# Kernel tuning notes

Hardware: AMD Instinct MI355X
Metric: run time of the kernel (lower is better)

The kernel has to match this reference:

```python
import jax, jax.numpy as jnp
import numpy as np

B, S, D, H = 4, 2048, 768, 12
HD = D // H  # head_dim = 64
NEG = 1e10
EPS = 1e-5

def setup_inputs() -> dict:
    key = jax.random.key(0)
    k1, k2, k3 = jax.random.split(key, 3)
    return {
        "context": jax.random.normal(k1, (B, S, D), dtype=jnp.float32),
        "pad_mask": jnp.ones((B, S), dtype=jnp.float32),
        "w_qkv": jax.random.normal(k2, (D, 3 * D), dtype=jnp.float32) * 0.02,
        "w_proj": jax.random.normal(k3, (D, D), dtype=jnp.float32) * (0.02 / np.sqrt(2.0 * 12)),
        "b_proj": jnp.zeros((D,), dtype=jnp.float32),
        "gamma": jnp.ones((D,), dtype=jnp.float32),
        "beta": jnp.zeros((D,), dtype=jnp.float32),
    }

def reference(context, pad_mask, w_qkv, w_proj, b_proj, gamma, beta):
    b, s, d = context.shape
    resid = context
    qkv = context @ w_qkv                       # [B,S,3D]
    q, k, v = jnp.split(qkv, 3, axis=-1)
    # [B,S,D] -> [B,H,S,HD]
    q = q.reshape(b, s, H, HD).transpose(0, 2, 1, 3)
    k = k.reshape(b, s, H, HD).transpose(0, 2, 1, 3)
    v = v.reshape(b, s, H, HD).transpose(0, 2, 1, 3)
    scores = jnp.einsum("bhqd,bhkd->bhqk", q, k) * (1.0 / np.sqrt(HD))
    m = pad_mask[:, None, None, :]              # [B,1,1,S]
    scores = scores * m - (1.0 - m) * NEG       # multiplicative mask + big negative
    attn = jax.nn.softmax(scores, axis=-1)      # dropout is identity at inference
    out = jnp.einsum("bhqk,bhkd->bhqd", attn, v)
    out = out.transpose(0, 2, 1, 3).reshape(b, s, d)
    out = out @ w_proj + b_proj
    x = out + resid
    mu = jnp.mean(x, axis=-1, keepdims=True)
    var = jnp.var(x, axis=-1, keepdims=True)
    return (x - mu) * jax.lax.rsqrt(var + EPS) * gamma + beta
```

## Files before the change

### kernel.cpp

```cpp
#include <hip/hip_runtime.h>

#define BB 4
#define SS 2048
#define DD 768
#define HH 12
#define HDD 64
#define BS (BB*SS)
#define NQKV (3*DD)
#define NEL (BS*DD)

typedef __attribute__((ext_vector_type(8))) __bf16 bf16x8;
typedef __attribute__((ext_vector_type(4))) float fx4;
typedef __attribute__((ext_vector_type(4))) int   ix4;

#define MFMA16(a,b,c) __builtin_amdgcn_mfma_f32_16x16x32_bf16((a),(b),(c),0,0,0)

#define GLLDS(g, l) __builtin_amdgcn_global_load_lds( \
    (const __attribute__((address_space(1))) void*)(g), \
    (__attribute__((address_space(3))) void*)(l), 16, 0, 0)

__device__ __forceinline__ unsigned short f2bf(float f) {
  unsigned u = __builtin_bit_cast(unsigned, f);
  u = (u + 0x7FFFu + ((u >> 16) & 1u)) >> 16;
  return (unsigned short)u;
}
__device__ __forceinline__ unsigned pkbf(float a, float b) {
  unsigned ua = __builtin_bit_cast(unsigned, a);
  unsigned ub = __builtin_bit_cast(unsigned, b);
  return ((ua + 0x8000u) >> 16) | ((ub + 0x8000u) & 0xFFFF0000u);
}
__device__ __forceinline__ unsigned cvtpk(float a, float b) {
  unsigned r;
  asm("v_cvt_pk_bf16_f32 %0, %1, %2" : "=v"(r) : "v"(a), "v"(b));
  return r;
}
__device__ __forceinline__ float ex2(float x) { return __builtin_amdgcn_exp2f(x); }

__global__ __launch_bounds__(256) void pack_bf16(const float* __restrict__ x,
                                                 unsigned short* __restrict__ y, int n4) {
  int i = blockIdx.x * 256 + threadIdx.x;
  if (i < n4) {
    float4 v = ((const float4*)x)[i];
    ((uint2*)y)[i] = make_uint2(pkbf(v.x, v.y), pkbf(v.z, v.w));
  }
}

__global__ __launch_bounds__(256) void pack_transpose(const float* __restrict__ w,
                                                      unsigned short* __restrict__ wT,
                                                      int K, int N) {
  __shared__ unsigned short t[32][33];
  int n0 = blockIdx.x * 32, k0 = blockIdx.y * 32;
  int tx = threadIdx.x & 31, ty = threadIdx.x >> 5;
#pragma unroll
  for (int r = ty; r < 32; r += 8)
    t[tx][r] = f2bf(w[(size_t)(k0 + r) * N + n0 + tx]);
  __syncthreads();
#pragma unroll
  for (int r = ty; r < 32; r += 8)
    wT[(size_t)(n0 + r) * K + k0 + tx] = t[r][tx];
}

__global__ __launch_bounds__(256) void gemm_qkv_k(const unsigned short* __restrict__ Wt,
                                                  const unsigned short* __restrict__ X,
                                                  unsigned short* __restrict__ Qo,
                                                  unsigned short* __restrict__ Ko,
                                                  unsigned short* __restrict__ Vto) {
  __shared__ unsigned short As[128 * 32];
  __shared__ unsigned short Bs[128 * 32];
  const int tid = threadIdx.x;
  const int w = tid >> 6, lane = tid & 63, quad = lane >> 4, l16 = lane & 15;
  const int m0 = blockIdx.y << 7;
  const int n0 = blockIdx.x << 7;
  const int wm = (w & 1) * 64, wn = (w >> 1) * 64;
  fx4 acc[4][4];
#pragma unroll
  for (int i = 0; i < 4; ++i)
#pragma unroll
    for (int c = 0; c < 4; ++c) acc[i][c] = (fx4){0.f, 0.f, 0.f, 0.f};

  const int c0 = tid, c1 = 256 + tid;
  const unsigned short* Ag0 = Wt + (size_t)(m0 + (c0 >> 2)) * DD + (c0 & 3) * 8;
  const unsigned short* Ag1 = Wt + (size_t)(m0 + (c1 >> 2)) * DD + (c1 & 3) * 8;
  const unsigned short* Bg0 = X + (size_t)(n0 + (c0 >> 2)) * DD + (c0 & 3) * 8;
  const unsigned short* Bg1 = X + (size_t)(n0 + (c1 >> 2)) * DD + (c1 & 3) * 8;
  const int wb = w * 1024;

  for (int k0 = 0; k0 < DD; k0 += 32) {
    GLLDS(Ag0 + k0, (char*)As + wb);
    GLLDS(Ag1 + k0, (char*)As + 4096 + wb);
    GLLDS(Bg0 + k0, (char*)Bs + wb);
    GLLDS(Bg1 + k0, (char*)Bs + 4096 + wb);
    __syncthreads();
    bf16x8 af[4], bf[4];
#pragma unroll
    for (int i = 0; i < 4; ++i) af[i] = *(const bf16x8*)&As[(wm + i * 16 + l16) * 32 + quad * 8];
#pragma unroll
    for (int c = 0; c < 4; ++c) bf[c] = *(const bf16x8*)&Bs[(wn + c * 16 + l16) * 32 + quad * 8];
#pragma unroll
    for (int i = 0; i < 4; ++i)
#pragma unroll
      for (int c = 0; c < 4; ++c) acc[i][c] = MFMA16(af[i], bf[c], acc[i][c]);
    __syncthreads();
  }

  const int which = m0 / DD;
#pragma unroll
  for (int i = 0; i < 4; ++i) {
    int fb = m0 + wm + i * 16 + quad * 4;
    int d = fb - which * DD;
    int h = d >> 6, hd = d & 63;
#pragma unroll
    for (int c = 0; c < 4; ++c) {
      int srow = n0 + wn + c * 16 + l16;
      int b = srow >> 11, s = srow & (SS - 1);
      if (which == 0) {
        uint2 v = make_uint2(pkbf(acc[i][c][0], acc[i][c][1]), pkbf(acc[i][c][2], acc[i][c][3]));
        *(uint2*)&Qo[((size_t)(b * HH + h) * SS + s) * HDD + hd] = v;
      } else if (which == 1) {
        uint2 v = make_uint2(pkbf(acc[i][c][0], acc[i][c][1]), pkbf(acc[i][c][2], acc[i][c][3]));
        *(uint2*)&Ko[((size_t)(b * HH + h) * SS + s) * HDD + hd] = v;
      } else {
#pragma unroll
        for (int r = 0; r < 4; ++r)
          Vto[((size_t)(b * HH + h) * HDD + hd + r) * SS + s] = f2bf(acc[i][c][r]);
      }
    }
  }
}

__global__ __launch_bounds__(256) void gemm_proj_k(const unsigned short* __restrict__ Wt,
                                                   const unsigned short* __restrict__ X,
                                                   const float* __restrict__ ctx,
                                                   const float* __restrict__ bproj,
                                                   float* __restrict__ xf) {
  __shared__ unsigned short As[128 * 32];
  __shared__ unsigned short Bs[128 * 32];
  const int tid = threadIdx.x;
  const int w = tid >> 6, lane = tid & 63, quad = lane >> 4, l16 = lane & 15;
  const int m0 = blockIdx.y << 7;
  const int n0 = blockIdx.x << 7;
  const int wm = (w & 1) * 64, wn = (w >> 1) * 64;
  fx4 acc[4][4];
#pragma unroll
  for (int i = 0; i < 4; ++i)
#pragma unroll
    for (int c = 0; c < 4; ++c) acc[i][c] = (fx4){0.f, 0.f, 0.f, 0.f};

  const int c0 = tid, c1 = 256 + tid;
  const unsigned short* Ag0 = Wt + (size_t)(m0 + (c0 >> 2)) * DD + (c0 & 3) * 8;
  const unsigned short* Ag1 = Wt + (size_t)(m0 + (c1 >> 2)) * DD + (c1 & 3) * 8;
  const unsigned short* Bg0 = X + (size_t)(n0 + (c0 >> 2)) * DD + (c0 & 3) * 8;
  const unsigned short* Bg1 = X + (size_t)(n0 + (c1 >> 2)) * DD + (c1 & 3) * 8;
  const int wb = w * 1024;

  for (int k0 = 0; k0 < DD; k0 += 32) {
    GLLDS(Ag0 + k0, (char*)As + wb);
    GLLDS(Ag1 + k0, (char*)As + 4096 + wb);
    GLLDS(Bg0 + k0, (char*)Bs + wb);
    GLLDS(Bg1 + k0, (char*)Bs + 4096 + wb);
    __syncthreads();
    bf16x8 af[4], bf[4];
#pragma unroll
    for (int i = 0; i < 4; ++i) af[i] = *(const bf16x8*)&As[(wm + i * 16 + l16) * 32 + quad * 8];
#pragma unroll
    for (int c = 0; c < 4; ++c) bf[c] = *(const bf16x8*)&Bs[(wn + c * 16 + l16) * 32 + quad * 8];
#pragma unroll
    for (int i = 0; i < 4; ++i)
#pragma unroll
      for (int c = 0; c < 4; ++c) acc[i][c] = MFMA16(af[i], bf[c], acc[i][c]);
    __syncthreads();
  }

#pragma unroll
  for (int i = 0; i < 4; ++i) {
    int fb = m0 + wm + i * 16 + quad * 4;
    float4 bp = *(const float4*)&bproj[fb];
#pragma unroll
    for (int c = 0; c < 4; ++c) {
      int srow = n0 + wn + c * 16 + l16;
      float4 cx = *(const float4*)&ctx[(size_t)srow * DD + fb];
      float4 r;
      r.x = acc[i][c][0] + bp.x + cx.x;
      r.y = acc[i][c][1] + bp.y + cx.y;
      r.z = acc[i][c][2] + bp.z + cx.z;
      r.w = acc[i][c][3] + bp.w + cx.w;
      *(float4*)&xf[(size_t)srow * DD + fb] = r;
    }
  }
}

__global__ __launch_bounds__(256) void attn_k(const unsigned short* __restrict__ Q,
                                              const unsigned short* __restrict__ K,
                                              const unsigned short* __restrict__ Vt,
                                              const float* __restrict__ mask,
                                              unsigned short* __restrict__ O) {
  __shared__ unsigned short Ks[64 * 64];
  __shared__ unsigned short Vts[64 * 64];
  const int tid = threadIdx.x;
  const int w = tid >> 6, lane = tid & 63;
  const int quad = lane >> 4, l16 = lane & 15;
  const int bh = blockIdx.y;
  const int b = bh / HH, h = bh - b * HH;
  const int q0 = blockIdx.x << 7;
  const unsigned short* Qb = Q + (size_t)bh * (SS * HDD);
  const unsigned short* Kb = K + (size_t)bh * (SS * HDD);
  const unsigned short* Vtb = Vt + (size_t)bh * (SS * HDD);
  const float* mb = mask + b * SS;

  bf16x8 qf[2][2];
#pragma unroll
  for (int qi = 0; qi < 2; ++qi)
#pragma unroll
    for (int f = 0; f < 2; ++f)
      qf[qi][f] = *(const bf16x8*)&Qb[(size_t)(q0 + w * 32 + qi * 16 + l16) * HDD + f * 32 + quad * 8];

  fx4 o[2][4];
#pragma unroll
  for (int qi = 0; qi < 2; ++qi)
#pragma unroll
    for (int ht = 0; ht < 4; ++ht) o[qi][ht] = (fx4){0.f, 0.f, 0.f, 0.f};
  fx4 sacc[2];
  sacc[0] = (fx4){0.f, 0.f, 0.f, 0.f};
  sacc[1] = (fx4){0.f, 0.f, 0.f, 0.f};

  const ix4 one4 = (ix4){0x3F803F80, 0x3F803F80, 0x3F803F80, 0x3F803F80};
  const bf16x8 onesf = __builtin_bit_cast(bf16x8, one4);

  const int cA = tid, cB = 256 + tid;
  const int rA = cA >> 3, pA = (cA & 7) ^ (rA & 7);
  const int rB = cB >> 3, pB = (cB & 7) ^ (rB & 7);

  ix4 rk0 = *(const ix4*)&Kb[(size_t)rA * HDD + pA * 8];
  ix4 rk1 = *(const ix4*)&Kb[(size_t)rB * HDD + pB * 8];
  ix4 rv0 = *(const ix4*)&Vtb[(size_t)rA * SS + pA * 8];
  ix4 rv1 = *(const ix4*)&Vtb[(size_t)rB * SS + pB * 8];

  for (int k0 = 0; k0 < SS; k0 += 64) {
    __syncthreads();
    *(ix4*)((char*)Ks + cA * 16) = rk0;
    *(ix4*)((char*)Ks + cB * 16) = rk1;
    *(ix4*)((char*)Vts + cA * 16) = rv0;
    *(ix4*)((char*)Vts + cB * 16) = rv1;
    __syncthreads();
    if (k0 + 64 < SS) {
      int kn = k0 + 64;
      rk0 = *(const ix4*)&Kb[(size_t)(kn + rA) * HDD + pA * 8];
      rk1 = *(const ix4*)&Kb[(size_t)(kn + rB) * HDD + pB * 8];
      rv0 = *(const ix4*)&Vtb[(size_t)rA * SS + kn + pA * 8];
      rv1 = *(const ix4*)&Vtb[(size_t)rB * SS + kn + pB * 8];
    }

    float4 mqa[4], mqb[4];
#pragma unroll
    for (int kt = 0; kt < 4; ++kt) {
      float4 mq = *(const float4*)&mb[k0 + kt * 16 + quad * 4];
      mqa[kt].x = mq.x * 0.18033688f;
      mqa[kt].y = mq.y * 0.18033688f;
      mqa[kt].z = mq.z * 0.18033688f;
      mqa[kt].w = mq.w * 0.18033688f;
      mqb[kt].x = __builtin_fmaf(mq.x, 1.44269504e10f, -1.44269504e10f);
      mqb[kt].y = __builtin_fmaf(mq.y, 1.44269504e10f, -1.44269504e10f);
      mqb[kt].z = __builtin_fmaf(mq.z, 1.44269504e10f, -1.44269504e10f);
      mqb[kt].w = __builtin_fmaf(mq.w, 1.44269504e10f, -1.44269504e10f);
    }

    bf16x8 kf[4][2];
#pragma unroll
    for (int kt = 0; kt < 4; ++kt) {
      int row = kt * 16 + l16;
      int rx = row & 7;
#pragma unroll
      for (int f = 0; f < 2; ++f)
        kf[kt][f] = *(const bf16x8*)&Ks[row * 64 + ((f * 4 + quad) ^ rx) * 8];
    }
    bf16x8 vf[4][2];
#pragma unroll
    for (int ht = 0; ht < 4; ++ht) {
      int row = ht * 16 + l16;
      int rx = row & 7;
#pragma unroll
      for (int f = 0; f < 2; ++f) {
        int dc0 = (f * 4 + (quad >> 1)) ^ rx;
        int dc1 = (f * 4 + 2 + (quad >> 1)) ^ rx;
        uint2 lo = *(const uint2*)((const char*)Vts + row * 128 + dc0 * 16 + (quad & 1) * 8);
        uint2 hi = *(const uint2*)((const char*)Vts + row * 128 + dc1 * 16 + (quad & 1) * 8);
        ix4 vv = (ix4){(int)lo.x, (int)lo.y, (int)hi.x, (int)hi.y};
        vf[ht][f] = __builtin_bit_cast(bf16x8, vv);
      }
    }

#pragma unroll
    for (int qi = 0; qi < 2; ++qi) {
      unsigned pw[8];
#pragma unroll
      for (int kt = 0; kt < 4; ++kt) {
        fx4 s = (fx4){0.f, 0.f, 0.f, 0.f};
        s = MFMA16(kf[kt][0], qf[qi][0], s);
        s = MFMA16(kf[kt][1], qf[qi][1], s);
        const float* ma = (const float*)&mqa[kt];
        const float* mc = (const float*)&mqb[kt];
        float p0 = ex2(__builtin_fmaf(s[0], ma[0], mc[0]));
        float p1 = ex2(__builtin_fmaf(s[1], ma[1], mc[1]));
        float p2 = ex2(__builtin_fmaf(s[2], ma[2], mc[2]));
        float p3 = ex2(__builtin_fmaf(s[3], ma[3], mc[3]));
        pw[kt * 2]     = cvtpk(p0, p1);
        pw[kt * 2 + 1] = cvtpk(p2, p3);
      }
      ix4 pi0 = (ix4){(int)pw[0], (int)pw[1], (int)pw[2], (int)pw[3]};
      ix4 pi1 = (ix4){(int)pw[4], (int)pw[5], (int)pw[6], (int)pw[7]};
      bf16x8 pf0 = __builtin_bit_cast(bf16x8, pi0);
      bf16x8 pf1 = __builtin_bit_cast(bf16x8, pi1);
      sacc[qi] = MFMA16(onesf, pf0, sacc[qi]);
      sacc[qi] = MFMA16(onesf, pf1, sacc[qi]);
#pragma unroll
      for (int ht = 0; ht < 4; ++ht) {
        o[qi][ht] = MFMA16(vf[ht][0], pf0, o[qi][ht]);
        o[qi][ht] = MFMA16(vf[ht][1], pf1, o[qi][ht]);
      }
    }
  }

#pragma unroll
  for (int qi = 0; qi < 2; ++qi) {
    float inv = 1.f / fmaxf(sacc[qi][0], 1e-30f);
    int sq = q0 + w * 32 + qi * 16 + l16;
    unsigned short* orow = O + ((size_t)(b * SS + sq)) * DD + h * HDD;
#pragma unroll
    for (int ht = 0; ht < 4; ++ht) {
      uint2 v = make_uint2(pkbf(o[qi][ht][0] * inv, o[qi][ht][1] * inv),
                           pkbf(o[qi][ht][2] * inv, o[qi][ht][3] * inv));
      *(uint2*)&orow[ht * 16 + quad * 4] = v;
    }
  }
}

__global__ __launch_bounds__(256) void ln_k(const float* __restrict__ x,
                                            const float* __restrict__ gamma,
                                            const float* __restrict__ beta,
                                            float* __restrict__ out) {
  const int row = blockIdx.x;
  const float* xr = x + (size_t)row * DD;
  const int t = threadIdx.x;
  float v0 = xr[t], v1 = xr[t + 256], v2 = xr[t + 512];
  float s = v0 + v1 + v2;
  float ss = v0 * v0 + v1 * v1 + v2 * v2;
#pragma unroll
  for (int d = 32; d > 0; d >>= 1) {
    s += __shfl_down(s, d);
    ss += __shfl_down(ss, d);
  }
  __shared__ float sh[10];
  int wv = t >> 6, lane = t & 63;
  if (lane == 0) { sh[wv] = s; sh[4 + wv] = ss; }
  __syncthreads();
  if (t == 0) {
    float S = sh[0] + sh[1] + sh[2] + sh[3];
    float SSm = sh[4] + sh[5] + sh[6] + sh[7];
    float mu = S * (1.0f / DD);
    float var = SSm * (1.0f / DD) - mu * mu;
    sh[8] = mu;
    sh[9] = rsqrtf(var + 1e-5f);
  }
  __syncthreads();
  float mu = sh[8], rstd = sh[9];
  out[(size_t)row * DD + t]       = (v0 - mu) * rstd * gamma[t]       + beta[t];
  out[(size_t)row * DD + t + 256] = (v1 - mu) * rstd * gamma[t + 256] + beta[t + 256];
  out[(size_t)row * DD + t + 512] = (v2 - mu) * rstd * gamma[t + 512] + beta[t + 512];
}

extern "C" void kernel_launch(void* const* d_in, const int* in_sizes, int n_in,
                              void* d_out, int out_size, void* d_ws, size_t ws_size,
                              hipStream_t stream) {
  (void)in_sizes; (void)n_in; (void)out_size; (void)ws_size;
  const float* ctx   = (const float*)d_in[0];
  const float* mask  = (const float*)d_in[1];
  const float* wqkv  = (const float*)d_in[2];
  const float* wproj = (const float*)d_in[3];
  const float* bproj = (const float*)d_in[4];
  const float* gamma = (const float*)d_in[5];
  const float* beta  = (const float*)d_in[6];
  float* out = (float*)d_out;

  char* p = (char*)d_ws;
  unsigned short* Xbf = (unsigned short*)p; p += (size_t)NEL * 2;
  unsigned short* Qw  = (unsigned short*)p; p += (size_t)NEL * 2;
  unsigned short* Kw  = (unsigned short*)p; p += (size_t)NEL * 2;
  unsigned short* Vtw = (unsigned short*)p; p += (size_t)NEL * 2;
  unsigned short* Ao  = (unsigned short*)p; p += (size_t)NEL * 2;
  unsigned short* WqkvT  = (unsigned short*)p; p += (size_t)DD * NQKV * 2;
  unsigned short* WprojT = (unsigned short*)p; p += (size_t)DD * DD * 2;
  float* xf = (float*)Qw;

  pack_bf16<<<NEL / 4 / 256, 256, 0, stream>>>(ctx, Xbf, NEL / 4);
  pack_transpose<<<dim3(NQKV / 32, DD / 32), 256, 0, stream>>>(wqkv, WqkvT, DD, NQKV);
  pack_transpose<<<dim3(DD / 32, DD / 32), 256, 0, stream>>>(wproj, WprojT, DD, DD);
  gemm_qkv_k<<<dim3(BS / 128, NQKV / 128), 256, 0, stream>>>(WqkvT, Xbf, Qw, Kw, Vtw);
  attn_k<<<dim3(SS / 128, BB * HH), 256, 0, stream>>>(Qw, Kw, Vtw, mask, Ao);
  gemm_proj_k<<<dim3(BS / 128, DD / 128), 256, 0, stream>>>(WprojT, Ao, ctx, bproj, xf);
  ln_k<<<BS, 256, 0, stream>>>(xf, gamma, beta, out);
}
```

Baseline: 258.6 us.

## Double-buffer LDS tiles via async global-to-LDS loads in GEMMs and attention

Both GEMM kernels and the attention kernel now use two LDS buffers. The next K tile is issued with global_load_lds while the current tile is consumed, which removes one barrier per iteration and overlaps memory latency with MFMA work. Attention drops its register-staged K/V copies in favour of direct global-to-LDS loads, raises wave priority around the MFMA/softmax section, and reads mask coefficients precomputed by a new small kernel. This doubles LDS use per block, which may lower occupancy, and adds one extra kernel launch.

Measured after the change: 277.7 us. +7.4%, slower.

```diff
diff --git a/kernel.cpp b/kernel.cpp
--- a/kernel.cpp
+++ b/kernel.cpp
@@ -45,6 +45,17 @@
   }
 }
 
+__global__ __launch_bounds__(256) void mask_coef_k(const float* __restrict__ m,
+                                                   float* __restrict__ ka,
+                                                   float* __restrict__ kb, int n) {
+  int i = blockIdx.x * 256 + threadIdx.x;
+  if (i < n) {
+    float v = m[i];
+    ka[i] = v * 0.18033688f;
+    kb[i] = __builtin_fmaf(v, 1.44269504e10f, -1.44269504e10f);
+  }
+}
+
 __global__ __launch_bounds__(256) void pack_transpose(const float* __restrict__ w,
                                                       unsigned short* __restrict__ wT,
                                                       int K, int N) {
@@ -65,8 +76,8 @@
                                                   unsigned short* __restrict__ Qo,
                                                   unsigned short* __restrict__ Ko,
                                                   unsigned short* __restrict__ Vto) {
-  __shared__ unsigned short As[128 * 32];
-  __shared__ unsigned short Bs[128 * 32];
+  __shared__ unsigned short As[2 * 128 * 32];
+  __shared__ unsigned short Bs[2 * 128 * 32];
   const int tid = threadIdx.x;
   const int w = tid >> 6, lane = tid & 63, quad = lane >> 4, l16 = lane & 15;
   const int m0 = blockIdx.y << 7;
@@ -85,22 +96,32 @@
   const unsigned short* Bg1 = X + (size_t)(n0 + (c1 >> 2)) * DD + (c1 & 3) * 8;
   const int wb = w * 1024;
 
+  GLLDS(Ag0, (char*)As + wb);
+  GLLDS(Ag1, (char*)As + 4096 + wb);
+  GLLDS(Bg0, (char*)Bs + wb);
+  GLLDS(Bg1, (char*)Bs + 4096 + wb);
+  int cur = 0;
+
   for (int k0 = 0; k0 < DD; k0 += 32) {
-    GLLDS(Ag0 + k0, (char*)As + wb);
-    GLLDS(Ag1 + k0, (char*)As + 4096 + wb);
-    GLLDS(Bg0 + k0, (char*)Bs + wb);
-    GLLDS(Bg1 + k0, (char*)Bs + 4096 + wb);
     __syncthreads();
+    if (k0 + 32 < DD) {
+      GLLDS(Ag0 + k0 + 32, (char*)As + (cur ^ 1) * 8192 + wb);
+      GLLDS(Ag1 + k0 + 32, (char*)As + (cur ^ 1) * 8192 + 4096 + wb);
+      GLLDS(Bg0 + k0 + 32, (char*)Bs + (cur ^ 1) * 8192 + wb);
+      GLLDS(Bg1 + k0 + 32, (char*)Bs + (cur ^ 1) * 8192 + 4096 + wb);
+    }
+    const unsigned short* Asc = As + cur * 4096;
+    const unsigned short* Bsc = Bs + cur * 4096;
     bf16x8 af[4], bf[4];
 #pragma unroll
-    for (int i = 0; i < 4; ++i) af[i] = *(const bf16x8*)&As[(wm + i * 16 + l16) * 32 + quad * 8];
-#pragma unroll
-    for (int c = 0; c < 4; ++c) bf[c] = *(const bf16x8*)&Bs[(wn + c * 16 + l16) * 32 + quad * 8];
+    for (int i = 0; i < 4; ++i) af[i] = *(const bf16x8*)&Asc[(wm + i * 16 + l16) * 32 + quad * 8];
+#pragma unroll
+    for (int c = 0; c < 4; ++c) bf[c] = *(const bf16x8*)&Bsc[(wn + c * 16 + l16) * 32 + quad * 8];
 #pragma unroll
     for (int i = 0; i < 4; ++i)
 #pragma unroll
       for (int c = 0; c < 4; ++c) acc[i][c] = MFMA16(af[i], bf[c], acc[i][c]);
-    __syncthreads();
+    cur ^= 1;
   }
 
   const int which = m0 / DD;
@@ -133,8 +154,8 @@
                                                    const float* __restrict__ ctx,
                                                    const float* __restrict__ bproj,
                                                    float* __restrict__ xf) {
-  __shared__ unsigned short As[128 * 32];
-  __shared__ unsigned short Bs[128 * 32];
+  __shared__ unsigned short As[2 * 128 * 32];
+  __shared__ unsigned short Bs[2 * 128 * 32];
   const int tid = threadIdx.x;
   const int w = tid >> 6, lane = tid & 63, quad = lane >> 4, l16 = lane & 15;
   const int m0 = blockIdx.y << 7;
@@ -153,22 +174,32 @@
   const unsigned short* Bg1 = X + (size_t)(n0 + (c1 >> 2)) * DD + (c1 & 3) * 8;
   const int wb = w * 1024;
 
+  GLLDS(Ag0, (char*)As + wb);
+  GLLDS(Ag1, (char*)As + 4096 + wb);
+  GLLDS(Bg0, (char*)Bs + wb);
+  GLLDS(Bg1, (char*)Bs + 4096 + wb);
+  int cur = 0;
+
   for (int k0 = 0; k0 < DD; k0 += 32) {
-    GLLDS(Ag0 + k0, (char*)As + wb);
-    GLLDS(Ag1 + k0, (char*)As + 4096 + wb);
-    GLLDS(Bg0 + k0, (char*)Bs + wb);
-    GLLDS(Bg1 + k0, (char*)Bs + 4096 + wb);
     __syncthreads();
+    if (k0 + 32 < DD) {
+      GLLDS(Ag0 + k0 + 32, (char*)As + (cur ^ 1) * 8192 + wb);
+      GLLDS(Ag1 + k0 + 32, (char*)As + (cur ^ 1) * 8192 + 4096 + wb);
+      GLLDS(Bg0 + k0 + 32, (char*)Bs + (cur ^ 1) * 8192 + wb);
+      GLLDS(Bg1 + k0 + 32, (char*)Bs + (cur ^ 1) * 8192 + 4096 + wb);
+    }
+    const unsigned short* Asc = As + cur * 4096;
+    const unsigned short* Bsc = Bs + cur * 4096;
     bf16x8 af[4], bf[4];
 #pragma unroll
-    for (int i = 0; i < 4; ++i) af[i] = *(const bf16x8*)&As[(wm + i * 16 + l16) * 32 + quad * 8];
-#pragma unroll
-    for (int c = 0; c < 4; ++c) bf[c] = *(const bf16x8*)&Bs[(wn + c * 16 + l16) * 32 + quad * 8];
+    for (int i = 0; i < 4; ++i) af[i] = *(const bf16x8*)&Asc[(wm + i * 16 + l16) * 32 + quad * 8];
+#pragma unroll
+    for (int c = 0; c < 4; ++c) bf[c] = *(const bf16x8*)&Bsc[(wn + c * 16 + l16) * 32 + quad * 8];
 #pragma unroll
     for (int i = 0; i < 4; ++i)
 #pragma unroll
       for (int c = 0; c < 4; ++c) acc[i][c] = MFMA16(af[i], bf[c], acc[i][c]);
-    __syncthreads();
+    cur ^= 1;
   }
 
 #pragma unroll
@@ -192,10 +223,11 @@
 __global__ __launch_bounds__(256) void attn_k(const unsigned short* __restrict__ Q,
                                               const unsigned short* __restrict__ K,
                                               const unsigned short* __restrict__ Vt,
-                                              const float* __restrict__ mask,
+                                              const float* __restrict__ ka,
+                                              const float* __restrict__ kb,
                                               unsigned short* __restrict__ O) {
-  __shared__ unsigned short Ks[64 * 64];
-  __shared__ unsigned short Vts[64 * 64];
+  __shared__ unsigned short Ks[2 * 64 * 64];
+  __shared__ unsigned short Vts[2 * 64 * 64];
   const int tid = threadIdx.x;
   const int w = tid >> 6, lane = tid & 63;
   const int quad = lane >> 4, l16 = lane & 15;
@@ -205,7 +237,8 @@
   const unsigned short* Qb = Q + (size_t)bh * (SS * HDD);
   const unsigned short* Kb = K + (size_t)bh * (SS * HDD);
   const unsigned short* Vtb = Vt + (size_t)bh * (SS * HDD);
-  const float* mb = mask + b * SS;
+  const float* ka_b = ka + b * SS;
+  const float* kb_b = kb + b * SS;
 
   bf16x8 qf[2][2];
 #pragma unroll
@@ -229,39 +262,36 @@
   const int cA = tid, cB = 256 + tid;
   const int rA = cA >> 3, pA = (cA & 7) ^ (rA & 7);
   const int rB = cB >> 3, pB = (cB & 7) ^ (rB & 7);
-
-  ix4 rk0 = *(const ix4*)&Kb[(size_t)rA * HDD + pA * 8];
-  ix4 rk1 = *(const ix4*)&Kb[(size_t)rB * HDD + pB * 8];
-  ix4 rv0 = *(const ix4*)&Vtb[(size_t)rA * SS + pA * 8];
-  ix4 rv1 = *(const ix4*)&Vtb[(size_t)rB * SS + pB * 8];
+  const unsigned short* kSrcA = Kb + (size_t)rA * HDD + pA * 8;
+  const unsigned short* kSrcB = Kb + (size_t)rB * HDD + pB * 8;
+  const unsigned short* vSrcA = Vtb + (size_t)rA * SS + pA * 8;
+  const unsigned short* vSrcB = Vtb + (size_t)rB * SS + pB * 8;
+  const int wbA = w * 1024;
+  const int wbB = 4096 + w * 1024;
+
+  GLLDS(kSrcA, (char*)Ks + wbA);
+  GLLDS(kSrcB, (char*)Ks + wbB);
+  GLLDS(vSrcA, (char*)Vts + wbA);
+  GLLDS(vSrcB, (char*)Vts + wbB);
+  int cur = 0;
 
   for (int k0 = 0; k0 < SS; k0 += 64) {
-    __syncthreads();
-    *(ix4*)((char*)Ks + cA * 16) = rk0;
-    *(ix4*)((char*)Ks + cB * 16) = rk1;
-    *(ix4*)((char*)Vts + cA * 16) = rv0;
-    *(ix4*)((char*)Vts + cB * 16) = rv1;
     __syncthreads();
     if (k0 + 64 < SS) {
       int kn = k0 + 64;
-      rk0 = *(const ix4*)&Kb[(size_t)(kn + rA) * HDD + pA * 8];
-      rk1 = *(const ix4*)&Kb[(size_t)(kn + rB) * HDD + pB * 8];
-      rv0 = *(const ix4*)&Vtb[(size_t)rA * SS + kn + pA * 8];
-      rv1 = *(const ix4*)&Vtb[(size_t)rB * SS + kn + pB * 8];
-    }
+      GLLDS(kSrcA + (size_t)kn * HDD, (char*)Ks + (cur ^ 1) * 8192 + wbA);
+      GLLDS(kSrcB + (size_t)kn * HDD, (char*)Ks + (cur ^ 1) * 8192 + wbB);
+      GLLDS(vSrcA + kn, (char*)Vts + (cur ^ 1) * 8192 + wbA);
+      GLLDS(vSrcB + kn, (char*)Vts + (cur ^ 1) * 8192 + wbB);
+    }
+    const unsigned short* Ksc = Ks + cur * 4096;
+    const char* Vtsc = (const char*)Vts + cur * 8192;
 
     float4 mqa[4], mqb[4];
 #pragma unroll
     for (int kt = 0; kt < 4; ++kt) {
-      float4 mq = *(const float4*)&mb[k0 + kt * 16 + quad * 4];
-      mqa[kt].x = mq.x * 0.18033688f;
-      mqa[kt].y = mq.y * 0.18033688f;
-      mqa[kt].z = mq.z * 0.18033688f;
-      mqa[kt].w = mq.w * 0.18033688f;
-      mqb[kt].x = __builtin_fmaf(mq.x, 1.44269504e10f, -1.44269504e10f);
-      mqb[kt].y = __builtin_fmaf(mq.y, 1.44269504e10f, -1.44269504e10f);
-      mqb[kt].z = __builtin_fmaf(mq.z, 1.44269504e10f, -1.44269504e10f);
-      mqb[kt].w = __builtin_fmaf(mq.w, 1.44269504e10f, -1.44269504e10f);
+      mqa[kt] = *(const float4*)&ka_b[k0 + kt * 16 + quad * 4];
+      mqb[kt] = *(const float4*)&kb_b[k0 + kt * 16 + quad * 4];
     }
 
     bf16x8 kf[4][2];
@@ -271,7 +301,7 @@
       int rx = row & 7;
 #pragma unroll
       for (int f = 0; f < 2; ++f)
-        kf[kt][f] = *(const bf16x8*)&Ks[row * 64 + ((f * 4 + quad) ^ rx) * 8];
+        kf[kt][f] = *(const bf16x8*)&Ksc[row * 64 + ((f * 4 + quad) ^ rx) * 8];
     }
     bf16x8 vf[4][2];
 #pragma unroll
@@ -282,13 +312,14 @@
       for (int f = 0; f < 2; ++f) {
         int dc0 = (f * 4 + (quad >> 1)) ^ rx;
         int dc1 = (f * 4 + 2 + (quad >> 1)) ^ rx;
-        uint2 lo = *(const uint2*)((const char*)Vts + row * 128 + dc0 * 16 + (quad & 1) * 8);
-        uint2 hi = *(const uint2*)((const char*)Vts + row * 128 + dc1 * 16 + (quad & 1) * 8);
+        uint2 lo = *(const uint2*)(Vtsc + row * 128 + dc0 * 16 + (quad & 1) * 8);
+        uint2 hi = *(const uint2*)(Vtsc + row * 128 + dc1 * 16 + (quad & 1) * 8);
         ix4 vv = (ix4){(int)lo.x, (int)lo.y, (int)hi.x, (int)hi.y};
         vf[ht][f] = __builtin_bit_cast(bf16x8, vv);
       }
     }
 
+    __builtin_amdgcn_s_setprio(1);
 #pragma unroll
     for (int qi = 0; qi < 2; ++qi) {
       unsigned pw[8];
@@ -318,6 +349,8 @@
         o[qi][ht] = MFMA16(vf[ht][1], pf1, o[qi][ht]);
       }
     }
+    __builtin_amdgcn_s_setprio(0);
+    cur ^= 1;
   }
 
 #pragma unroll
@@ -389,13 +422,16 @@
   unsigned short* Ao  = (unsigned short*)p; p += (size_t)NEL * 2;
   unsigned short* WqkvT  = (unsigned short*)p; p += (size_t)DD * NQKV * 2;
   unsigned short* WprojT = (unsigned short*)p; p += (size_t)DD * DD * 2;
+  float* kaw = (float*)p; p += (size_t)BS * 4;
+  float* kbw = (float*)p; p += (size_t)BS * 4;
   float* xf = (float*)Qw;
 
   pack_bf16<<<NEL / 4 / 256, 256, 0, stream>>>(ctx, Xbf, NEL / 4);
+  mask_coef_k<<<BS / 256, 256, 0, stream>>>(mask, kaw, kbw, BS);
   pack_transpose<<<dim3(NQKV / 32, DD / 32), 256, 0, stream>>>(wqkv, WqkvT, DD, NQKV);
   pack_transpose<<<dim3(DD / 32, DD / 32), 256, 0, stream>>>(wproj, WprojT, DD, DD);
   gemm_qkv_k<<<dim3(BS / 128, NQKV / 128), 256, 0, stream>>>(WqkvT, Xbf, Qw, Kw, Vtw);
-  attn_k<<<dim3(SS / 128, BB * HH), 256, 0, stream>>>(Qw, Kw, Vtw, mask, Ao);
+  attn_k<<<dim3(SS / 128, BB * HH), 256, 0, stream>>>(Qw, Kw, Vtw, kaw, kbw, Ao);
   gemm_proj_k<<<dim3(BS / 128, DD / 128), 256, 0, stream>>>(WprojT, Ao, ctx, bproj, xf);
   ln_k<<<BS, 256, 0, stream>>>(xf, gamma, beta, out);
 }
```
